# Kernel optimization log

Measured on AMD Instinct MI355X. Metric: run time of the kernel, lower is better.

The kernel has to match this reference:

```python
import jax, jax.numpy as jnp
import numpy as np

N_NODES = 20000
N_EDGES = 320000  # directed edges, in reverse pairs (2*i, 2*i+1)
F_NODE = 64
F_EDGE = 16
HID = 300
DEPTH = 3
N_GRAPHS = 128


def setup_inputs() -> dict:
    key = jax.random.key(0)
    ks = jax.random.split(key, 16)
    x = jax.random.normal(ks[0], (N_NODES, F_NODE), dtype=jnp.float32)
    edge_attr = jax.random.normal(ks[1], (N_EDGES, F_EDGE), dtype=jnp.float32)
    # build paired directed edges: edge 2*i is (src,dst), edge 2*i+1 is (dst,src)
    half = N_EDGES // 2
    src = jax.random.randint(ks[2], (half,), 0, N_NODES)
    dst = jax.random.randint(ks[3], (half,), 0, N_NODES)
    row = jnp.stack([src, dst], axis=1).reshape(-1)  # [E]
    col = jnp.stack([dst, src], axis=1).reshape(-1)  # [E]
    edge_index = jnp.stack([row, col], axis=0)  # [2, E]
    batch = jnp.sort(jax.random.randint(ks[4], (N_NODES,), 0, N_GRAPHS))
    s = 0.05
    W_init = jax.random.normal(ks[5], (F_NODE + F_EDGE, HID), dtype=jnp.float32) * s
    b_init = jnp.zeros((HID,), dtype=jnp.float32)
    W_convs = jax.random.normal(ks[6], (DEPTH, HID, HID), dtype=jnp.float32) * s
    b_convs = jnp.zeros((DEPTH, HID), dtype=jnp.float32)
    W_e2n = jax.random.normal(ks[7], (F_NODE + HID, HID), dtype=jnp.float32) * s
    b_e2n = jnp.zeros((HID,), dtype=jnp.float32)
    W_ffn = jax.random.normal(ks[8], (HID, 1), dtype=jnp.float32) * s
    b_ffn = jnp.zeros((1,), dtype=jnp.float32)
    return {"x": x, "edge_attr": edge_attr, "edge_index": edge_index, "batch": batch,
            "W_init": W_init, "b_init": b_init, "W_convs": W_convs, "b_convs": b_convs,
            "W_e2n": W_e2n, "b_e2n": b_e2n, "W_ffn": W_ffn, "b_ffn": b_ffn}


def _rev(h):
    # swap each consecutive forward/reverse edge pair
    e = h.shape[0]
    return h.reshape(e // 2, 2, -1)[:, ::-1, :].reshape(e, -1)


def reference(x, edge_attr, edge_index, batch, W_init, b_init, W_convs, b_convs,
              W_e2n, b_e2n, W_ffn, b_ffn):
    row, col = edge_index[0], edge_index[1]
    # h_0 = act(edge_init(cat([x[row], edge_attr])))
    h0 = jax.nn.relu(jnp.concatenate([x[row], edge_attr], axis=1) @ W_init + b_init)
    h = h0
    for l in range(DEPTH):
        # DMPNNConv: scatter-add edge features to target nodes, gather at source,
        # subtract reverse-edge message, apply Linear
        a = jax.ops.segment_sum(h, col, num_segments=N_NODES)  # [N, H]
        h = (a[row] - _rev(h)) @ W_convs[l] + b_convs[l]
        h = jax.nn.relu(h + h0)  # skip then activation; dropout is eval no-op
    # final conv's a_message only
    s = jax.ops.segment_sum(h, col, num_segments=N_NODES)  # [N, H]
    q = jnp.concatenate([x, s], axis=1)
    hn = jax.nn.relu(q @ W_e2n + b_e2n)  # [N, H]
    pooled = jax.ops.segment_sum(hn, batch, num_segments=N_GRAPHS)  # [G, H]
    return (pooled @ W_ffn + b_ffn).squeeze(-1)  # [G]
```

## Files before the change

### kernel.cpp

```cpp
#include <hip/hip_runtime.h>
#include <hip/hip_bf16.h>

typedef unsigned short ushort_t;
typedef __attribute__((ext_vector_type(8))) short short8;
typedef __attribute__((ext_vector_type(4))) float f32x4;
typedef __attribute__((ext_vector_type(2))) float f32x2;

#define N_NODES 20000
#define N_EDGES 320000
#define F_NODE 64
#define F_EDGE 16
#define HID 300
#define HP 300
#define NTILES 20
#define DEPTH 3
#define N_GRAPHS 128
#define KE2N 384
#define ATS 328

#define WFRAG_USHORT_PER_LAYER (10 * NTILES * 64 * 8)
#define W2FRAG_USHORT (NTILES * 64 * 8)
#define WE2NFRAG_USHORT (12 * NTILES * 64 * 8)


__device__ __forceinline__ float bf2f(ushort_t u) {
    union { unsigned int i; float f; } v;
    v.i = ((unsigned int)u) << 16;
    return v.f;
}

__device__ __forceinline__ f32x2 bfpair(unsigned int u) {
    union { unsigned int i[2]; f32x2 f; } v;
    v.i[0] = u << 16;
    v.i[1] = u & 0xffff0000u;
    return v.f;
}

__device__ __forceinline__ f32x2 pmax0(f32x2 a) {
#if __has_builtin(__builtin_elementwise_max)
    f32x2 z = {0.f, 0.f};
    return __builtin_elementwise_max(a, z);
#else
    f32x2 r; r.x = fmaxf(a.x, 0.f); r.y = fmaxf(a.y, 0.f); return r;
#endif
}

__device__ __forceinline__ unsigned int fpack(float lo, float hi) {
#if __has_builtin(__builtin_amdgcn_cvt_pk_bf16_f32)
    auto r = __builtin_amdgcn_cvt_pk_bf16_f32(lo, hi);
    union { decltype(r) b; unsigned int u; } v;
    v.b = r;
    return v.u;
#else
    union { float f; unsigned int i; } a, b;
    a.f = lo; b.f = hi;
    return ((a.i + 0x8000u) >> 16) | ((b.i + 0x8000u) & 0xffff0000u);
#endif
}
__device__ __forceinline__ unsigned int fpack2(f32x2 a) { return fpack(a.x, a.y); }
__device__ __forceinline__ ushort_t f2bf(float f) {
    return (ushort_t)(fpack(f, 0.f) & 0xffffu);
}

__global__ __launch_bounds__(256) void csr_hist(
    const int* __restrict__ col, int* __restrict__ deg)
{
    int e = blockIdx.x * 256 + threadIdx.x;
    atomicAdd(&deg[col[e]], 1);
}

__global__ __launch_bounds__(256) void csr_scan(
    const int* __restrict__ deg, int* __restrict__ offsets,
    int* __restrict__ cursor)
{
    __shared__ int sums[256];
    const int t = threadIdx.x;
    const int CH = 79;
    int base = t * CH;
    int local = 0;
    for (int i = 0; i < CH; ++i) {
        int idx = base + i;
        if (idx < N_NODES) local += deg[idx];
    }
    sums[t] = local;
    __syncthreads();
    for (int off = 1; off < 256; off <<= 1) {
        int v = (t >= off) ? sums[t - off] : 0;
        __syncthreads();
        sums[t] += v;
        __syncthreads();
    }
    int run = (t > 0) ? sums[t - 1] : 0;
    for (int i = 0; i < CH; ++i) {
        int idx = base + i;
        if (idx < N_NODES) {
            offsets[idx] = run;
            cursor[idx] = run;
            run += deg[idx];
        }
    }
}

__global__ __launch_bounds__(256) void csr_fill(
    const int* __restrict__ col, int* __restrict__ cursor,
    int* __restrict__ eid)
{
    int e = blockIdx.x * 256 + threadIdx.x;
    int pos = atomicAdd(&cursor[col[e]], 1);
    eid[pos] = e;
}

__global__ __launch_bounds__(256) void ghist(
    const int* __restrict__ batch, int* __restrict__ gdeg)
{
    int n = blockIdx.x * 256 + threadIdx.x;
    if (n < N_NODES) atomicAdd(&gdeg[batch[n]], 1);
}

__global__ __launch_bounds__(128) void gscan(
    const int* __restrict__ gdeg, int* __restrict__ goff)
{
    __shared__ int s[128];
    int t = threadIdx.x;
    int d = gdeg[t];
    s[t] = d;
    __syncthreads();
    for (int off = 1; off < 128; off <<= 1) {
        int v = (t >= off) ? s[t - off] : 0;
        __syncthreads();
        s[t] += v;
        __syncthreads();
    }
    goff[t] = s[t] - d;
    if (t == 127) goff[128] = s[127];
}

__global__ __launch_bounds__(64) void wfrag_build(
    const float* __restrict__ W_convs, ushort_t* __restrict__ wfrag)
{
    const int c = blockIdx.x, t = blockIdx.y, l = blockIdx.z;
    const int lane = threadIdx.x;
    const int k0 = c * 32 + (lane >> 4) * 8;
    const int n  = t * 16 + (lane & 15);
    ushort_t* dst = wfrag + (size_t)l * WFRAG_USHORT_PER_LAYER
                  + ((size_t)(c * NTILES + t) * 64 + lane) * 8;
    const float* Wl = W_convs + (size_t)l * HID * HID;
    #pragma unroll
    for (int j = 0; j < 8; ++j) {
        int k = k0 + j;
        float v = (k < HID && n < HID) ? Wl[(long)k * HID + n] : 0.f;
        dst[j] = f2bf(v);
    }
}

__global__ __launch_bounds__(64) void wfrag2_build(
    const float* __restrict__ W_e2n, ushort_t* __restrict__ wfrag2)
{
    const int c = blockIdx.x, t = blockIdx.y;
    const int lane = threadIdx.x;
    const int k0 = c * 32 + (lane >> 4) * 8;
    const int n  = t * 16 + (lane & 15);
    ushort_t* dst = wfrag2 + ((size_t)(c * NTILES + t) * 64 + lane) * 8;
    #pragma unroll
    for (int j = 0; j < 8; ++j) {
        int k = k0 + j;
        float v = (k < F_NODE + HID && n < HID) ? W_e2n[(long)k * HID + n] : 0.f;
        dst[j] = f2bf(v);
    }
}

__global__ __launch_bounds__(64) void w2frag_build(
    const float* __restrict__ W2, ushort_t* __restrict__ w2frag)
{
    const int t = blockIdx.x;
    const int lane = threadIdx.x;
    const int k0 = (lane >> 4) * 8;
    const int n  = t * 16 + (lane & 15);
    ushort_t* dst = w2frag + ((size_t)t * 64 + lane) * 8;
    #pragma unroll
    for (int j = 0; j < 8; ++j) {
        int k = k0 + j;
        float v = (k < F_EDGE && n < HID) ? W2[(long)k * HID + n] : 0.f;
        dst[j] = f2bf(v);
    }
}


__global__ __launch_bounds__(256) void node_init_gemm(
    const float* __restrict__ x, const float* __restrict__ W_init,
    const float* __restrict__ b_init, ushort_t* __restrict__ xW1b)
{
    __shared__ float xs[16 * 64];
    const int tid = threadIdx.x;
    const long n0 = (long)blockIdx.x * 16;
    for (int i = tid; i < 16 * 64; i += 256) xs[i] = x[n0 * 64 + i];
    __syncthreads();
    const int nl = tid >> 4, ct = tid & 15;
    for (int q = 0; q < 19; ++q) {
        int c = ct + 16 * q;
        if (c < HID) {
            float acc = b_init[c];
            #pragma unroll 8
            for (int k = 0; k < 64; ++k)
                acc = fmaf(xs[nl * 64 + k], W_init[(long)k * HID + c], acc);
            xW1b[(n0 + nl) * HID + c] = f2bf(acc);
        }
    }
}

__device__ __forceinline__ void p_phase8(
    ushort_t* At, const float* __restrict__ edge_attr,
    const ushort_t* __restrict__ w2frag, long e0,
    int wave, int quad, int m, int lane)
{
    const int mtp = wave >> 2;
    const int nt0p = (wave & 3) * 5;
    short8 a_ea;
    {
        union { uint4 u4; short8 s8; } af;
        if (quad < 2) {
            const float* eap = edge_attr + (e0 + mtp * 16 + m) * 16 + quad * 8;
            float4 v0 = *(const float4*)eap;
            float4 v1 = *(const float4*)(eap + 4);
            af.u4.x = fpack(v0.x, v0.y); af.u4.y = fpack(v0.z, v0.w);
            af.u4.z = fpack(v1.x, v1.y); af.u4.w = fpack(v1.z, v1.w);
        } else {
            af.u4.x = 0; af.u4.y = 0; af.u4.z = 0; af.u4.w = 0;
        }
        a_ea = af.s8;
    }
    #pragma unroll
    for (int t = 0; t < 5; ++t) {
        short8 b = *(const short8*)(w2frag + ((size_t)(nt0p + t) * 64 + lane) * 8);
        int c = (nt0p + t) * 16 + m;
        f32x4 pc = (f32x4){0.f, 0.f, 0.f, 0.f};
        pc = __builtin_amdgcn_mfma_f32_16x16x32_bf16(a_ea, b, pc, 0, 0, 0);
        #pragma unroll
        for (int r = 0; r < 4; ++r)
            At[(mtp * 16 + quad * 4 + r) * ATS + c] = f2bf(pc[r]);
    }
}

template<bool UPDATE>
__global__ __launch_bounds__(256) void fused_conv(
    ushort_t* h, const ushort_t* __restrict__ Sb,
    const ushort_t* __restrict__ xW1b, const float* __restrict__ edge_attr,
    const int* __restrict__ row, const ushort_t* __restrict__ w2frag,
    const ushort_t* __restrict__ wfrag_l)
{
    __shared__ ushort_t At[32 * ATS];
    __shared__ int rows[32];
    const int tid = threadIdx.x;
    const int wave = tid >> 6, lane = tid & 63;
    const int quad = lane >> 4, m = lane & 15;
    const long e0 = (long)blockIdx.x * 32;
    if (tid < 32) rows[tid] = row[e0 + tid];

    {
        short8 a_ea[2];
        #pragma unroll
        for (int mt = 0; mt < 2; ++mt) {
            union { uint4 u4; short8 s8; } af;
            if (quad < 2) {
                const float* eap = edge_attr + (e0 + mt * 16 + m) * 16 + quad * 8;
                float4 v0 = *(const float4*)eap;
                float4 v1 = *(const float4*)(eap + 4);
                af.u4.x = fpack(v0.x, v0.y); af.u4.y = fpack(v0.z, v0.w);
                af.u4.z = fpack(v1.x, v1.y); af.u4.w = fpack(v1.z, v1.w);
            } else {
                af.u4.x = 0; af.u4.y = 0; af.u4.z = 0; af.u4.w = 0;
            }
            a_ea[mt] = af.s8;
        }
        const int nt0 = wave * 5;
        #pragma unroll
        for (int t = 0; t < 5; ++t) {
            short8 b = *(const short8*)(w2frag + ((size_t)(nt0 + t) * 64 + lane) * 8);
            int c = (nt0 + t) * 16 + m;
            #pragma unroll
            for (int mt = 0; mt < 2; ++mt) {
                f32x4 pc = (f32x4){0.f, 0.f, 0.f, 0.f};
                pc = __builtin_amdgcn_mfma_f32_16x16x32_bf16(a_ea[mt], b, pc, 0, 0, 0);
                #pragma unroll
                for (int r = 0; r < 4; ++r)
                    At[(mt * 16 + quad * 4 + r) * ATS + c] = f2bf(pc[r]);
            }
        }
    }
    __syncthreads();

    for (int i = tid; i < 16 * 80; i += 256) {
        int p = i / 80, g = i % 80;
        int c0 = 4 * g;
        int la = 2 * p, lb = 2 * p + 1;
        uint2 oa, ob;
        if (g < 75) {
            long Ea = e0 + la, Eb = e0 + lb;
            int ra = rows[la], rb = rows[lb];
            uint2 xa = *(const uint2*)&xW1b[(long)ra * HID + c0];
            uint2 xb = *(const uint2*)&xW1b[(long)rb * HID + c0];
            uint2 pa = *(const uint2*)&At[la * ATS + c0];
            uint2 pb = *(const uint2*)&At[lb * ATS + c0];
            f32x2 h0a0 = pmax0(bfpair(xa.x) + bfpair(pa.x));
            f32x2 h0a1 = pmax0(bfpair(xa.y) + bfpair(pa.y));
            f32x2 h0b0 = pmax0(bfpair(xb.x) + bfpair(pb.x));
            f32x2 h0b1 = pmax0(bfpair(xb.y) + bfpair(pb.y));
            if (UPDATE) {
                uint2 wa = *(const uint2*)&h[Ea * HP + c0];
                uint2 wb = *(const uint2*)&h[Eb * HP + c0];
                uint2 sa = *(const uint2*)&Sb[(long)ra * HID + c0];
                uint2 sb = *(const uint2*)&Sb[(long)rb * HID + c0];
                oa.x = fpack2(pmax0(bfpair(sa.x) - bfpair(wb.x) + h0a0));
                oa.y = fpack2(pmax0(bfpair(sa.y) - bfpair(wb.y) + h0a1));
                ob.x = fpack2(pmax0(bfpair(sb.x) - bfpair(wa.x) + h0b0));
                ob.y = fpack2(pmax0(bfpair(sb.y) - bfpair(wa.y) + h0b1));
            } else {
                oa.x = fpack2(h0a0); oa.y = fpack2(h0a1);
                ob.x = fpack2(h0b0); ob.y = fpack2(h0b1);
            }
        } else {
            oa.x = 0; oa.y = 0;
            ob = oa;
        }
        *(uint2*)&At[la * ATS + c0] = oa;
        *(uint2*)&At[lb * ATS + c0] = ob;
    }
    __syncthreads();

    const int nt0 = wave * 5;
    f32x4 acc[5][2];
    #pragma unroll
    for (int t = 0; t < 5; ++t)
        #pragma unroll
        for (int mt = 0; mt < 2; ++mt)
            acc[t][mt] = (f32x4){0.f, 0.f, 0.f, 0.f};

    for (int c = 0; c < 10; ++c) {
        short8 a[2];
        #pragma unroll
        for (int mt = 0; mt < 2; ++mt)
            a[mt] = *(const short8*)&At[(mt * 16 + m) * ATS + c * 32 + quad * 8];
        #pragma unroll
        for (int t = 0; t < 5; ++t) {
            short8 b = *(const short8*)(wfrag_l
                + ((size_t)(c * NTILES + nt0 + t) * 64 + lane) * 8);
            #pragma unroll
            for (int mt = 0; mt < 2; ++mt)
                acc[t][mt] = __builtin_amdgcn_mfma_f32_16x16x32_bf16(
                    a[mt], b, acc[t][mt], 0, 0, 0);
        }
    }
    #pragma unroll
    for (int t = 0; t < 5; ++t) {
        int col = (nt0 + t) * 16 + m;
        if (col >= HID) continue;
        #pragma unroll
        for (int mt = 0; mt < 2; ++mt) {
            long rbase = (e0 + mt * 16 + quad * 4) * HP + col;
            #pragma unroll
            for (int r = 0; r < 4; ++r)
                h[rbase + (long)r * HP] = f2bf(acc[t][mt][r]);
        }
    }
}

__global__ __launch_bounds__(512) void edge_update_mfma(
    ushort_t* h, const ushort_t* __restrict__ Sb,
    const ushort_t* __restrict__ xW1b, const float* __restrict__ edge_attr,
    const int* __restrict__ row, const ushort_t* __restrict__ w2frag)
{
    __shared__ ushort_t Pt[32 * ATS];
    const int tid = threadIdx.x;
    const int wave = tid >> 6, lane = tid & 63;
    const int quad = lane >> 4, m = lane & 15;
    const long e0 = (long)blockIdx.x * 32;

    auto issue = [&](int k, uint2& xa, uint2& xb, uint2& wa, uint2& wb,
                     uint2& sa, uint2& sb, int& la, int& lb, int& g, bool& v) {
        int i = tid + (k << 9);
        v = i < 16 * 75;
        if (v) {
            int p = i / 75; g = i % 75;
            la = 2 * p; lb = la + 1;
            int c0 = 4 * g;
            int ra = row[e0 + la], rb = row[e0 + lb];
            xa = *(const uint2*)&xW1b[(long)ra * HID + c0];
            xb = *(const uint2*)&xW1b[(long)rb * HID + c0];
            wa = *(const uint2*)&h[(e0 + la) * HP + c0];
            wb = *(const uint2*)&h[(e0 + lb) * HP + c0];
            sa = *(const uint2*)&Sb[(long)ra * HID + c0];
            sb = *(const uint2*)&Sb[(long)rb * HID + c0];
        }
    };

    uint2 xa0, xb0, wa0, wb0, sa0, sb0;
    int la0 = 0, lb0 = 0, g0 = 0; bool v0 = false;
    issue(0, xa0, xb0, wa0, wb0, sa0, sb0, la0, lb0, g0, v0);

    p_phase8(Pt, edge_attr, w2frag, e0, wave, quad, m, lane);
    __syncthreads();

    #pragma unroll
    for (int k = 0; k < 3; ++k) {
        uint2 xa1, xb1, wa1, wb1, sa1, sb1;
        int la1 = 0, lb1 = 0, g1 = 0; bool v1 = false;
        if (k < 2)
            issue(k + 1, xa1, xb1, wa1, wb1, sa1, sb1, la1, lb1, g1, v1);
        if (v0) {
            int c0 = 4 * g0;
            uint2 pa = *(const uint2*)&Pt[la0 * ATS + c0];
            uint2 pb = *(const uint2*)&Pt[lb0 * ATS + c0];
            f32x2 h0a0 = pmax0(bfpair(xa0.x) + bfpair(pa.x));
            f32x2 h0a1 = pmax0(bfpair(xa0.y) + bfpair(pa.y));
            f32x2 h0b0 = pmax0(bfpair(xb0.x) + bfpair(pb.x));
            f32x2 h0b1 = pmax0(bfpair(xb0.y) + bfpair(pb.y));
            uint2 oa, ob;
            oa.x = fpack2(pmax0(bfpair(sa0.x) - bfpair(wb0.x) + h0a0));
            oa.y = fpack2(pmax0(bfpair(sa0.y) - bfpair(wb0.y) + h0a1));
            ob.x = fpack2(pmax0(bfpair(sb0.x) - bfpair(wa0.x) + h0b0));
            ob.y = fpack2(pmax0(bfpair(sb0.y) - bfpair(wa0.y) + h0b1));
            *(uint2*)&h[(e0 + la0) * HP + c0] = oa;
            *(uint2*)&h[(e0 + lb0) * HP + c0] = ob;
        }
        if (k < 2) {
            xa0 = xa1; xb0 = xb1; wa0 = wa1; wb0 = wb1;
            sa0 = sa1; sb0 = sb1; la0 = la1; lb0 = lb1; g0 = g1; v0 = v1;
        }
    }
}

__global__ __launch_bounds__(256) void gather_sum(
    const ushort_t* __restrict__ src, const int* __restrict__ offsets,
    const int* __restrict__ ends, const int* __restrict__ eid,
    const float* __restrict__ bias, ushort_t* __restrict__ Sb)
{
    long idx = (long)blockIdx.x * 256 + threadIdx.x;
    if (idx >= (long)N_NODES * 75) return;
    int n = (int)(idx / 75);
    int g = (int)(idx % 75);
    int beg = offsets[n], end = ends[n];
    f32x2 A0 = {0.f, 0.f}, A1 = {0.f, 0.f};
    f32x2 B0 = {0.f, 0.f}, B1 = {0.f, 0.f};
    f32x2 C0 = {0.f, 0.f}, C1 = {0.f, 0.f};
    f32x2 D0 = {0.f, 0.f}, D1 = {0.f, 0.f};
    int j = beg;
    for (; j + 3 < end; j += 4) {
        int ea = eid[j], eb = eid[j + 1], ec = eid[j + 2], ed = eid[j + 3];
        uint2 va = ((const uint2*)src)[(long)ea * (HP / 4) + g];
        uint2 vb = ((const uint2*)src)[(long)eb * (HP / 4) + g];
        uint2 vc = ((const uint2*)src)[(long)ec * (HP / 4) + g];
        uint2 vd = ((const uint2*)src)[(long)ed * (HP / 4) + g];
        A0 += bfpair(va.x); A1 += bfpair(va.y);
        B0 += bfpair(vb.x); B1 += bfpair(vb.y);
        C0 += bfpair(vc.x); C1 += bfpair(vc.y);
        D0 += bfpair(vd.x); D1 += bfpair(vd.y);
    }
    for (; j < end; ++j) {
        int ea = eid[j];
        uint2 va = ((const uint2*)src)[(long)ea * (HP / 4) + g];
        A0 += bfpair(va.x); A1 += bfpair(va.y);
    }
    float4 bv = *(const float4*)&bias[4 * g];
    f32x2 bv0 = {bv.x, bv.y}, bv1 = {bv.z, bv.w};
    uint2 o;
    o.x = fpack2((A0 + B0) + (C0 + D0) + bv0);
    o.y = fpack2((A1 + B1) + (C1 + D1) + bv1);
    *(uint2*)&Sb[(long)n * HID + 4 * g] = o;
}

__global__ __launch_bounds__(256) void gather_ab(
    const ushort_t* __restrict__ src, const int* __restrict__ offsets,
    const int* __restrict__ ends, const int* __restrict__ eid,
    ushort_t* __restrict__ Ab)
{
    long idx = (long)blockIdx.x * 256 + threadIdx.x;
    if (idx >= (long)N_NODES * 75) return;
    int n = (int)(idx / 75);
    int g = (int)(idx % 75);
    int beg = offsets[n], end = ends[n];
    f32x2 A0 = {0.f, 0.f}, A1 = {0.f, 0.f};
    f32x2 B0 = {0.f, 0.f}, B1 = {0.f, 0.f};
    f32x2 C0 = {0.f, 0.f}, C1 = {0.f, 0.f};
    f32x2 D0 = {0.f, 0.f}, D1 = {0.f, 0.f};
    int j = beg;
    for (; j + 3 < end; j += 4) {
        int ea = eid[j], eb = eid[j + 1], ec = eid[j + 2], ed = eid[j + 3];
        uint2 va = ((const uint2*)src)[(long)ea * (HP / 4) + g];
        uint2 vb = ((const uint2*)src)[(long)eb * (HP / 4) + g];
        uint2 vc = ((const uint2*)src)[(long)ec * (HP / 4) + g];
        uint2 vd = ((const uint2*)src)[(long)ed * (HP / 4) + g];
        A0 += bfpair(va.x); A1 += bfpair(va.y);
        B0 += bfpair(vb.x); B1 += bfpair(vb.y);
        C0 += bfpair(vc.x); C1 += bfpair(vc.y);
        D0 += bfpair(vd.x); D1 += bfpair(vd.y);
    }
    for (; j < end; ++j) {
        int ea = eid[j];
        uint2 va = ((const uint2*)src)[(long)ea * (HP / 4) + g];
        A0 += bfpair(va.x); A1 += bfpair(va.y);
    }
    uint2 o;
    o.x = fpack2((A0 + B0) + (C0 + D0));
    o.y = fpack2((A1 + B1) + (C1 + D1));
    *(uint2*)&Ab[(long)n * KE2N + 64 + 4 * g] = o;
}

__global__ __launch_bounds__(256) void x_fill(
    const float* __restrict__ x, ushort_t* __restrict__ Ab)
{
    long idx = (long)blockIdx.x * 256 + threadIdx.x;
    if (idx >= (long)N_NODES * 21) return;
    int n = (int)(idx / 21);
    int q = (int)(idx % 21);
    if (q < 16) {
        float4 v = *(const float4*)&x[(long)n * 64 + 4 * q];
        uint2 o;
        o.x = fpack(v.x, v.y);
        o.y = fpack(v.z, v.w);
        *(uint2*)&Ab[(long)n * KE2N + 4 * q] = o;
    } else {
        uint2 o; o.x = 0; o.y = 0;
        *(uint2*)&Ab[(long)n * KE2N + 364 + 4 * (q - 16)] = o;
    }
}

__global__ __launch_bounds__(256) void e2n_mfma(
    const ushort_t* __restrict__ Ab, const ushort_t* __restrict__ wfrag2,
    const float* __restrict__ b_e2n, float* __restrict__ hn)
{
    const int tid = threadIdx.x;
    const int wave = tid >> 6, lane = tid & 63;
    const int quad = lane >> 4, m = lane & 15;
    const long n0 = (long)blockIdx.x * 32;
    const int nt0 = wave * 5;

    f32x4 acc[5][2];
    #pragma unroll
    for (int t = 0; t < 5; ++t)
        #pragma unroll
        for (int mt = 0; mt < 2; ++mt)
            acc[t][mt] = (f32x4){0.f, 0.f, 0.f, 0.f};

    for (int c = 0; c < 12; ++c) {
        short8 a[2];
        #pragma unroll
        for (int mt = 0; mt < 2; ++mt) {
            long r = n0 + mt * 16 + m;
            a[mt] = *(const short8*)(Ab + r * KE2N + c * 32 + quad * 8);
        }
        #pragma unroll
        for (int t = 0; t < 5; ++t) {
            short8 b = *(const short8*)(wfrag2
                + ((size_t)(c * NTILES + nt0 + t) * 64 + lane) * 8);
            #pragma unroll
            for (int mt = 0; mt < 2; ++mt)
                acc[t][mt] = __builtin_amdgcn_mfma_f32_16x16x32_bf16(
                    a[mt], b, acc[t][mt], 0, 0, 0);
        }
    }

    #pragma unroll
    for (int t = 0; t < 5; ++t) {
        int col = (nt0 + t) * 16 + m;
        if (col >= HID) continue;
        float bias = b_e2n[col];
        #pragma unroll
        for (int mt = 0; mt < 2; ++mt) {
            long rw = n0 + mt * 16 + quad * 4;
            #pragma unroll
            for (int r = 0; r < 4; ++r)
                hn[(rw + r) * HP + col] = fmaxf(acc[t][mt][r] + bias, 0.f);
        }
    }
}

__global__ __launch_bounds__(256) void pool_graph(
    const float* __restrict__ hn, const int* __restrict__ goff,
    float* __restrict__ pooled)
{
    int g = blockIdx.x;
    int beg = goff[g], end = goff[g + 1];
    for (int c = threadIdx.x; c < HID; c += 256) {
        float acc = 0.f;
        for (int n = beg; n < end; ++n)
            acc += hn[(long)n * HP + c];
        pooled[(long)g * HID + c] = acc;
    }
}

__global__ __launch_bounds__(64) void ffn_out(
    const float* __restrict__ pooled, const float* __restrict__ W_ffn,
    const float* __restrict__ b_ffn, float* __restrict__ out)
{
    int g = blockIdx.x;
    int lane = threadIdx.x;
    float s = 0.f;
    for (int c = lane; c < HID; c += 64)
        s += pooled[(long)g * HID + c] * W_ffn[c];
    #pragma unroll
    for (int off = 32; off > 0; off >>= 1)
        s += __shfl_down(s, off, 64);
    if (lane == 0) out[g] = s + b_ffn[0];
}

extern "C" void kernel_launch(void* const* d_in, const int* in_sizes, int n_in,
                              void* d_out, int out_size, void* d_ws, size_t ws_size,
                              hipStream_t stream) {
    const float* x         = (const float*)d_in[0];
    const float* edge_attr = (const float*)d_in[1];
    const int*   edge_index= (const int*)d_in[2];
    const int*   batch     = (const int*)d_in[3];
    const float* W_init    = (const float*)d_in[4];
    const float* b_init    = (const float*)d_in[5];
    const float* W_convs   = (const float*)d_in[6];
    const float* b_convs   = (const float*)d_in[7];
    const float* W_e2n     = (const float*)d_in[8];
    const float* b_e2n     = (const float*)d_in[9];
    const float* W_ffn     = (const float*)d_in[10];
    const float* b_ffn     = (const float*)d_in[11];
    float* out = (float*)d_out;

    const int* row = edge_index;
    const int* col = edge_index + N_EDGES;
    const float* W2 = W_init + (size_t)F_NODE * HID;

    const size_t need = (size_t)N_EDGES * HP * 2
                      + (size_t)N_NODES * HID * 2
                      + (size_t)N_NODES * KE2N * 2
                      + (size_t)N_GRAPHS * HID * 4
                      + (size_t)N_NODES * 4 * 2 + (size_t)N_EDGES * 4
                      + (size_t)DEPTH * WFRAG_USHORT_PER_LAYER * 2
                      + (size_t)WE2NFRAG_USHORT * 2
                      + (size_t)W2FRAG_USHORT * 2
                      + (size_t)(N_GRAPHS + 1 + N_GRAPHS) * 4 + 32768;
    if (ws_size < need) return;

    char* p = (char*)d_ws;
    auto take = [&](size_t bytes) {
        char* q = p;
        p += (bytes + 255) & ~(size_t)255;
        return q;
    };
    ushort_t* h       = (ushort_t*)take((size_t)N_EDGES * HP * 2);
    ushort_t* Sb      = (ushort_t*)take((size_t)N_NODES * HID * 2);
    ushort_t* Ab      = (ushort_t*)take((size_t)N_NODES * KE2N * 2);
    float*    pooled  = (float*)take((size_t)N_GRAPHS * HID * 4);
    int*      cursor  = (int*)take((size_t)N_NODES * 4);
    int*      offsets = (int*)take((size_t)N_NODES * 4);
    int*      eid     = (int*)take((size_t)N_EDGES * 4);
    ushort_t* wfrag   = (ushort_t*)take((size_t)DEPTH * WFRAG_USHORT_PER_LAYER * 2);
    ushort_t* wfrag2  = (ushort_t*)take((size_t)WE2NFRAG_USHORT * 2);
    ushort_t* w2frag  = (ushort_t*)take((size_t)W2FRAG_USHORT * 2);
    int*      gdeg    = (int*)take((size_t)N_GRAPHS * 4);
    int*      goff    = (int*)take((size_t)(N_GRAPHS + 1) * 4);

    ushort_t* xW1b = Ab;
    float*    hn   = (float*)h;

    hipMemsetAsync(cursor, 0, (size_t)N_NODES * 4, stream);
    hipMemsetAsync(gdeg, 0, (size_t)N_GRAPHS * 4, stream);
    csr_hist<<<N_EDGES / 256, 256, 0, stream>>>(col, cursor);
    csr_scan<<<1, 256, 0, stream>>>(cursor, offsets, cursor);
    csr_fill<<<N_EDGES / 256, 256, 0, stream>>>(col, cursor, eid);
    ghist<<<(N_NODES + 255) / 256, 256, 0, stream>>>(batch, gdeg);
    gscan<<<1, 128, 0, stream>>>(gdeg, goff);

    wfrag_build<<<dim3(10, NTILES, DEPTH), 64, 0, stream>>>(W_convs, wfrag);
    wfrag2_build<<<dim3(12, NTILES, 1), 64, 0, stream>>>(W_e2n, wfrag2);
    w2frag_build<<<NTILES, 64, 0, stream>>>(W2, w2frag);

    node_init_gemm<<<N_NODES / 16, 256, 0, stream>>>(x, W_init, b_init, xW1b);

    const int GS_GRID = ((N_NODES * 75) + 255) / 256;

    fused_conv<false><<<N_EDGES / 32, 256, 0, stream>>>(
        h, Sb, xW1b, edge_attr, row, w2frag, wfrag);
    gather_sum<<<GS_GRID, 256, 0, stream>>>(
        h, offsets, cursor, eid, b_convs + 0 * HID, Sb);
    fused_conv<true><<<N_EDGES / 32, 256, 0, stream>>>(
        h, Sb, xW1b, edge_attr, row, w2frag,
        wfrag + 1 * (size_t)WFRAG_USHORT_PER_LAYER);
    gather_sum<<<GS_GRID, 256, 0, stream>>>(
        h, offsets, cursor, eid, b_convs + 1 * HID, Sb);
    fused_conv<true><<<N_EDGES / 32, 256, 0, stream>>>(
        h, Sb, xW1b, edge_attr, row, w2frag,
        wfrag + 2 * (size_t)WFRAG_USHORT_PER_LAYER);
    gather_sum<<<GS_GRID, 256, 0, stream>>>(
        h, offsets, cursor, eid, b_convs + 2 * HID, Sb);
    edge_update_mfma<<<N_EDGES / 32, 512, 0, stream>>>(
        h, Sb, xW1b, edge_attr, row, w2frag);

    x_fill<<<((N_NODES * 21) + 255) / 256, 256, 0, stream>>>(x, Ab);
    gather_ab<<<GS_GRID, 256, 0, stream>>>(h, offsets, cursor, eid, Ab);
    e2n_mfma<<<N_NODES / 32, 256, 0, stream>>>(Ab, wfrag2, b_e2n, hn);
    pool_graph<<<N_GRAPHS, 256, 0, stream>>>(hn, goff, pooled);
    ffn_out<<<N_GRAPHS, 64, 0, stream>>>(pooled, W_ffn, b_ffn, out);
}
```

Measured before the change: 1.216 ms.

## Pad edge and node feature rows to 304 and split conv GEMM into two passes

Sets the row pitch of the edge hidden buffer h and the node sum buffer Sb to 304 elements instead of 300, so each 608-byte row starts on a 32-byte boundary and accesses are better aligned. It also splits the per-wave 5-tile MFMA accumulation in fused_conv into a 3-tile pass and a 2-tile pass, which lowers accumulator register pressure and may improve occupancy. In exchange the A tile is read from shared memory twice, and the padding adds about 1.3% more memory footprint.

```diff
diff --git a/kernel.cpp b/kernel.cpp
--- a/kernel.cpp
+++ b/kernel.cpp
@@ -11,7 +11,8 @@
 #define F_NODE 64
 #define F_EDGE 16
 #define HID 300
-#define HP 300
+#define HP 304
+#define SBP 304
 #define NTILES 20
 #define DEPTH 3
 #define N_GRAPHS 128
@@ -238,6 +239,48 @@
         #pragma unroll
         for (int r = 0; r < 4; ++r)
             At[(mtp * 16 + quad * 4 + r) * ATS + c] = f2bf(pc[r]);
+    }
+}
+
+template<int T0, int NT>
+__device__ __forceinline__ void conv_p2pass(
+    const ushort_t* At, const ushort_t* __restrict__ wfrag_l,
+    ushort_t* h, long e0, int nt0, int quad, int m, int lane)
+{
+    f32x4 acc[NT][2];
+    #pragma unroll
+    for (int t = 0; t < NT; ++t)
+        #pragma unroll
+        for (int mt = 0; mt < 2; ++mt)
+            acc[t][mt] = (f32x4){0.f, 0.f, 0.f, 0.f};
+
+    for (int c = 0; c < 10; ++c) {
+        short8 a[2];
+        #pragma unroll
+        for (int mt = 0; mt < 2; ++mt)
+            a[mt] = *(const short8*)&At[(mt * 16 + m) * ATS + c * 32 + quad * 8];
+        #pragma unroll
+        for (int t = 0; t < NT; ++t) {
+            short8 b = *(const short8*)(wfrag_l
+                + ((size_t)(c * NTILES + nt0 + T0 + t) * 64 + lane) * 8);
+            #pragma unroll
+            for (int mt = 0; mt < 2; ++mt)
+                acc[t][mt] = __builtin_amdgcn_mfma_f32_16x16x32_bf16(
+                    a[mt], b, acc[t][mt], 0, 0, 0);
+        }
+    }
+    #pragma unroll
+    for (int t = 0; t < NT; ++t) {
+        int col = (nt0 + T0 + t) * 16 + m;
+        if (col < HID) {
+            #pragma unroll
+            for (int mt = 0; mt < 2; ++mt) {
+                long rbase = (e0 + mt * 16 + quad * 4) * HP + col;
+                #pragma unroll
+                for (int r = 0; r < 4; ++r)
+                    h[rbase + (long)r * HP] = f2bf(acc[t][mt][r]);
+            }
+        }
     }
 }
 
@@ -308,8 +351,8 @@
             if (UPDATE) {
                 uint2 wa = *(const uint2*)&h[Ea * HP + c0];
                 uint2 wb = *(const uint2*)&h[Eb * HP + c0];
-                uint2 sa = *(const uint2*)&Sb[(long)ra * HID + c0];
-                uint2 sb = *(const uint2*)&Sb[(long)rb * HID + c0];
+                uint2 sa = *(const uint2*)&Sb[(long)ra * SBP + c0];
+                uint2 sb = *(const uint2*)&Sb[(long)rb * SBP + c0];
                 oa.x = fpack2(pmax0(bfpair(sa.x) - bfpair(wb.x) + h0a0));
                 oa.y = fpack2(pmax0(bfpair(sa.y) - bfpair(wb.y) + h0a1));
                 ob.x = fpack2(pmax0(bfpair(sb.x) - bfpair(wa.x) + h0b0));
@@ -328,40 +371,8 @@
     __syncthreads();
 
     const int nt0 = wave * 5;
-    f32x4 acc[5][2];
-    #pragma unroll
-    for (int t = 0; t < 5; ++t)
-        #pragma unroll
-        for (int mt = 0; mt < 2; ++mt)
-            acc[t][mt] = (f32x4){0.f, 0.f, 0.f, 0.f};
-
-    for (int c = 0; c < 10; ++c) {
-        short8 a[2];
-        #pragma unroll
-        for (int mt = 0; mt < 2; ++mt)
-            a[mt] = *(const short8*)&At[(mt * 16 + m) * ATS + c * 32 + quad * 8];
-        #pragma unroll
-        for (int t = 0; t < 5; ++t) {
-            short8 b = *(const short8*)(wfrag_l
-                + ((size_t)(c * NTILES + nt0 + t) * 64 + lane) * 8);
-            #pragma unroll
-            for (int mt = 0; mt < 2; ++mt)
-                acc[t][mt] = __builtin_amdgcn_mfma_f32_16x16x32_bf16(
-                    a[mt], b, acc[t][mt], 0, 0, 0);
-        }
-    }
-    #pragma unroll
-    for (int t = 0; t < 5; ++t) {
-        int col = (nt0 + t) * 16 + m;
-        if (col >= HID) continue;
-        #pragma unroll
-        for (int mt = 0; mt < 2; ++mt) {
-            long rbase = (e0 + mt * 16 + quad * 4) * HP + col;
-            #pragma unroll
-            for (int r = 0; r < 4; ++r)
-                h[rbase + (long)r * HP] = f2bf(acc[t][mt][r]);
-        }
-    }
+    conv_p2pass<0, 3>(At, wfrag_l, h, e0, nt0, quad, m, lane);
+    conv_p2pass<3, 2>(At, wfrag_l, h, e0, nt0, quad, m, lane);
 }
 
 __global__ __launch_bounds__(512) void edge_update_mfma(
@@ -388,8 +399,8 @@
             xb = *(const uint2*)&xW1b[(long)rb * HID + c0];
             wa = *(const uint2*)&h[(e0 + la) * HP + c0];
             wb = *(const uint2*)&h[(e0 + lb) * HP + c0];
-            sa = *(const uint2*)&Sb[(long)ra * HID + c0];
-            sb = *(const uint2*)&Sb[(long)rb * HID + c0];
+            sa = *(const uint2*)&Sb[(long)ra * SBP + c0];
+            sb = *(const uint2*)&Sb[(long)rb * SBP + c0];
         }
     };
 
@@ -465,7 +476,7 @@
     uint2 o;
     o.x = fpack2((A0 + B0) + (C0 + D0) + bv0);
     o.y = fpack2((A1 + B1) + (C1 + D1) + bv1);
-    *(uint2*)&Sb[(long)n * HID + 4 * g] = o;
+    *(uint2*)&Sb[(long)n * SBP + 4 * g] = o;
 }
 
 __global__ __launch_bounds__(256) void gather_ab(
@@ -625,7 +636,7 @@
     const float* W2 = W_init + (size_t)F_NODE * HID;
 
     const size_t need = (size_t)N_EDGES * HP * 2
-                      + (size_t)N_NODES * HID * 2
+                      + (size_t)N_NODES * SBP * 2
                       + (size_t)N_NODES * KE2N * 2
                       + (size_t)N_GRAPHS * HID * 4
                       + (size_t)N_NODES * 4 * 2 + (size_t)N_EDGES * 4
@@ -642,7 +653,7 @@
         return q;
     };
     ushort_t* h       = (ushort_t*)take((size_t)N_EDGES * HP * 2);
-    ushort_t* Sb      = (ushort_t*)take((size_t)N_NODES * HID * 2);
+    ushort_t* Sb      = (ushort_t*)take((size_t)N_NODES * SBP * 2);
     ushort_t* Ab      = (ushort_t*)take((size_t)N_NODES * KE2N * 2);
     float*    pooled  = (float*)take((size_t)N_GRAPHS * HID * 4);
     int*      cursor  = (int*)take((size_t)N_NODES * 4);
```

Result: slower. 1.350 ms (+11.0%).
